# Optimization experiments

Hardware: AMD Instinct MI355X
Metric: run time of the kernel (lower is better)

## Reference

```python
import jax, jax.numpy as jnp
import numpy as np

B, S, DD, DE, DA = 32, 2048, 1024, 1024, 1024
NEG = -1000000000.0


def setup_inputs() -> dict:
    key = jax.random.key(0)
    k1, k2, k3, k4, k5 = jax.random.split(key, 5)
    query_state = jax.random.normal(k1, (B, DD), dtype=jnp.float32)
    encoder_hidden_states = jax.random.normal(k2, (B, S, DE), dtype=jnp.float32)
    attention_mask = jax.random.randint(k3, (B, S), 0, 2, dtype=jnp.int32)
    # W_c: Linear(DD+DE -> DA, bias=False): weight shape [DA, DD+DE]
    W_c = jax.random.normal(k4, (DA, DD + DE), dtype=jnp.float32) / np.sqrt(DD + DE)
    # V: Linear(DA -> 1, bias=False): weight shape [1, DA]
    V = jax.random.normal(k5, (1, DA), dtype=jnp.float32) / np.sqrt(DA)
    return {
        "query_state": query_state,
        "encoder_hidden_states": encoder_hidden_states,
        "attention_mask": attention_mask,
        "W_c": W_c,
        "V": V,
    }


def reference(query_state, encoder_hidden_states, attention_mask, W_c, V):
    # Split W_c along input dim: cat([q, e]) @ W_c.T == q @ Wq.T + e @ We.T
    Wq = W_c[:, :DD]          # [DA, DD]
    We = W_c[:, DD:]          # [DA, DE]
    q_proj = jnp.einsum('bd,ad->ba', query_state, Wq)            # [B, DA]
    e_proj = jnp.einsum('bsd,ad->bsa', encoder_hidden_states, We)  # [B, S, DA]
    energies = jnp.tanh(q_proj[:, None, :] + e_proj)             # [B, S, DA]
    scores = jnp.einsum('bsa,a->bs', energies, V[0])             # [B, S]
    scores = jnp.where(attention_mask == 0, NEG, scores)
    attention_weights = jax.nn.softmax(scores, axis=1)           # [B, S]
    context_vector = jnp.einsum('bs,bsd->bd', attention_weights, encoder_hidden_states)
    return context_vector, attention_weights
```

## Files before the change

kernel.cpp:

```cpp
#include <hip/hip_runtime.h>
#include <hip/hip_bf16.h>

#define NB 32
#define NS 2048
#define NDD 1024
#define NDE 1024
#define NDA 1024
#define NEGV (-1000000000.0f)

typedef __attribute__((ext_vector_type(8))) __bf16 bf16x8;
typedef __attribute__((ext_vector_type(4))) float f32x4;

__device__ __forceinline__ float fast_tanh(float x) {
    x = fminf(10.0f, fmaxf(-10.0f, x));
    float e = __expf(2.0f * x);
    return __fdividef(e - 1.0f, e + 1.0f);
}

__device__ __forceinline__ float bfu2f(unsigned short v) {
    union { unsigned u; float f; } c; c.u = (unsigned)v << 16; return c.f;
}

__global__ void prep_we(const float* __restrict__ Wc, __bf16* __restrict__ We) {
    int f = blockIdx.x * 256 + threadIdx.x;
    int a  = f >> 8;
    int k4 = f & 255;
    float4 v = *reinterpret_cast<const float4*>(Wc + (size_t)a * (NDD + NDE) + NDD + k4 * 4);
    union { __bf16 h[4]; uint2 u; } pk;
    pk.h[0] = (__bf16)v.x; pk.h[1] = (__bf16)v.y;
    pk.h[2] = (__bf16)v.z; pk.h[3] = (__bf16)v.w;
    *reinterpret_cast<uint2*>(We + (size_t)a * NDE + k4 * 4) = pk.u;
}

__global__ void prep_e(const float* __restrict__ E, __bf16* __restrict__ Eb) {
    size_t i = ((size_t)blockIdx.x * 256 + threadIdx.x) * 8;
    f32x4 x = __builtin_nontemporal_load(reinterpret_cast<const f32x4*>(E + i));
    f32x4 y = __builtin_nontemporal_load(reinterpret_cast<const f32x4*>(E + i + 4));
    union { __bf16 h[8]; uint4 u; } pk;
    pk.h[0] = (__bf16)x[0]; pk.h[1] = (__bf16)x[1]; pk.h[2] = (__bf16)x[2]; pk.h[3] = (__bf16)x[3];
    pk.h[4] = (__bf16)y[0]; pk.h[5] = (__bf16)y[1]; pk.h[6] = (__bf16)y[2]; pk.h[7] = (__bf16)y[3];
    *reinterpret_cast<uint4*>(Eb + i) = pk.u;
}

__global__ void qproj_kernel(const float* __restrict__ q, const float* __restrict__ Wc,
                             float* __restrict__ qp) {
    __shared__ float qs[NDD];
    int b = blockIdx.y;
    int a = blockIdx.x * 256 + threadIdx.x;
    float4 qv = *reinterpret_cast<const float4*>(q + (size_t)b * NDD + threadIdx.x * 4);
    *reinterpret_cast<float4*>(qs + threadIdx.x * 4) = qv;
    __syncthreads();
    const float* wrow = Wc + (size_t)a * (NDD + NDE);
    float acc = 0.f;
#pragma unroll 4
    for (int k4 = 0; k4 < 256; ++k4) {
        float4 w = *reinterpret_cast<const float4*>(wrow + k4 * 4);
        acc += qs[k4*4+0] * w.x + qs[k4*4+1] * w.y + qs[k4*4+2] * w.z + qs[k4*4+3] * w.w;
    }
    qp[(size_t)b * NDA + a] = acc;
}

__global__ __launch_bounds__(512, 2) void score256(
    const __bf16* __restrict__ Eb, const __bf16* __restrict__ We,
    const float* __restrict__ qp, const float* __restrict__ Vv,
    float* __restrict__ sp) {
    __shared__ __align__(16) __bf16 As[2][256 * 64];
    __shared__ __align__(16) __bf16 Bs[2][256 * 64];

    const int tid  = threadIdx.x;
    const int lane = tid & 63;
    const int l15  = lane & 15;
    const int h    = lane >> 4;
    const int wid  = tid >> 6;
    const int wr   = wid >> 2;
    const int wc   = wid & 3;

    const int bid = blockIdx.x;
    const int xcd = bid & 7;
    const int j   = bid >> 3;
    const int m   = xcd * 32 + (j >> 2);
    const int n   = j & 3;
    const int row0  = m * 256;
    const int ncol0 = n * 256;
    const int b     = m >> 3;

    f32x4 acc[8][4];
#pragma unroll
    for (int mf = 0; mf < 8; ++mf)
#pragma unroll
        for (int nf = 0; nf < 4; ++nf)
            acc[mf][nf] = (f32x4){0.f, 0.f, 0.f, 0.f};

    int offE[4], offW[4];
#pragma unroll
    for (int i = 0; i < 4; ++i) {
        int rr = i * 64 + (tid >> 3);
        int sg = (tid & 7) ^ (rr & 7);
        offE[i] = (row0  + rr) * 1024 + sg * 8;
        offW[i] = (ncol0 + rr) * 1024 + sg * 8;
    }

    const int slot0 = ((h ^ (l15 & 7)) * 16);
    const int aoffl = (wr * 128 + l15) * 128 + slot0;
    const int boffl = (wc * 64  + l15) * 128 + slot0;

#define STAGE8(abuf, bbuf, kc)                                                          \
    {                                                                                   \
        _Pragma("unroll")                                                               \
        for (int i = 0; i < 4; ++i)                                                     \
            __builtin_amdgcn_global_load_lds(                                           \
                (const __attribute__((address_space(1))) unsigned*)(Eb + offE[i] + (kc)),\
                (__attribute__((address_space(3))) unsigned*)((char*)(abuf) + i * 8192 + wid * 1024), \
                16, 0, 0);                                                              \
        _Pragma("unroll")                                                               \
        for (int i = 0; i < 4; ++i)                                                     \
            __builtin_amdgcn_global_load_lds(                                           \
                (const __attribute__((address_space(1))) unsigned*)(We + offW[i] + (kc)),\
                (__attribute__((address_space(3))) unsigned*)((char*)(bbuf) + i * 8192 + wid * 1024), \
                16, 0, 0);                                                              \
    }

    STAGE8(&As[0][0], &Bs[0][0], 0)
    __syncthreads();

    for (int T = 0; T < 16; ++T) {
        const int cur = T & 1;
        const char* Ab = (const char*)&As[cur][0];
        const char* Bb = (const char*)&Bs[cur][0];
        if (T < 15) STAGE8(&As[cur ^ 1][0], &Bs[cur ^ 1][0], (T + 1) * 64)

        bf16x8 bfr[4][2], afr[4][2];
#pragma unroll
        for (int nf = 0; nf < 4; ++nf) {
            bfr[nf][0] = *reinterpret_cast<const bf16x8*>(Bb + (boffl + nf * 2048));
            bfr[nf][1] = *reinterpret_cast<const bf16x8*>(Bb + ((boffl + nf * 2048) ^ 64));
        }
#pragma unroll
        for (int mi = 0; mi < 4; ++mi) {
            afr[mi][0] = *reinterpret_cast<const bf16x8*>(Ab + (aoffl + mi * 2048));
            afr[mi][1] = *reinterpret_cast<const bf16x8*>(Ab + ((aoffl + mi * 2048) ^ 64));
        }
        __builtin_amdgcn_s_setprio(1);
#pragma unroll
        for (int ks = 0; ks < 2; ++ks)
#pragma unroll
            for (int mi = 0; mi < 4; ++mi)
#pragma unroll
                for (int nf = 0; nf < 4; ++nf)
                    acc[mi][nf] = __builtin_amdgcn_mfma_f32_16x16x32_bf16(afr[mi][ks], bfr[nf][ks], acc[mi][nf], 0, 0, 0);
        __builtin_amdgcn_s_setprio(0);
#pragma unroll
        for (int mi = 0; mi < 4; ++mi) {
            afr[mi][0] = *reinterpret_cast<const bf16x8*>(Ab + (aoffl + (4 + mi) * 2048));
            afr[mi][1] = *reinterpret_cast<const bf16x8*>(Ab + ((aoffl + (4 + mi) * 2048) ^ 64));
        }
        __builtin_amdgcn_s_setprio(1);
#pragma unroll
        for (int ks = 0; ks < 2; ++ks)
#pragma unroll
            for (int mi = 0; mi < 4; ++mi)
#pragma unroll
                for (int nf = 0; nf < 4; ++nf)
                    acc[4 + mi][nf] = __builtin_amdgcn_mfma_f32_16x16x32_bf16(afr[mi][ks], bfr[nf][ks], acc[4 + mi][nf], 0, 0, 0);
        __builtin_amdgcn_s_setprio(0);
        __syncthreads();
    }

    float qv[4], vv[4];
#pragma unroll
    for (int nf = 0; nf < 4; ++nf) {
        int col = ncol0 + wc * 64 + nf * 16 + l15;
        qv[nf] = qp[(size_t)b * NDA + col];
        vv[nf] = Vv[col];
    }
    float* ps2 = reinterpret_cast<float*>(&As[0][0]);
#pragma unroll
    for (int mf = 0; mf < 8; ++mf)
#pragma unroll
        for (int jj = 0; jj < 4; ++jj) {
            float s = 0.f;
#pragma unroll
            for (int nf = 0; nf < 4; ++nf)
                s += fast_tanh(qv[nf] + acc[mf][nf][jj]) * vv[nf];
            s += __shfl_xor(s, 1);
            s += __shfl_xor(s, 2);
            s += __shfl_xor(s, 4);
            s += __shfl_xor(s, 8);
            if (l15 == 0)
                ps2[(wr * 128 + mf * 16 + h * 4 + jj) * 4 + wc] = s;
        }
    __syncthreads();
    if (tid < 256)
        sp[(size_t)n * (NB * NS) + row0 + tid] =
            ps2[tid * 4] + ps2[tid * 4 + 1] + ps2[tid * 4 + 2] + ps2[tid * 4 + 3];
}

__global__ void softmax_kernel(const float* __restrict__ sp, const int* __restrict__ mask,
                               float* __restrict__ wout, int np) {
    int b = blockIdx.x;
    const int* mrow = mask + (size_t)b * NS;
    float v[8];
    float lmax = -INFINITY;
#pragma unroll
    for (int jj = 0; jj < 8; ++jj) {
        int s = threadIdx.x + 256 * jj;
        float sc = 0.f;
        for (int nn = 0; nn < np; ++nn) sc += sp[(size_t)nn * (NB * NS) + b * NS + s];
        v[jj] = (mrow[s] == 0) ? NEGV : sc;
        lmax = fmaxf(lmax, v[jj]);
    }
#pragma unroll
    for (int mm = 1; mm <= 32; mm <<= 1) lmax = fmaxf(lmax, __shfl_xor(lmax, mm));
    __shared__ float redm[4], reds[4];
    if ((threadIdx.x & 63) == 0) redm[threadIdx.x >> 6] = lmax;
    __syncthreads();
    float bmax = fmaxf(fmaxf(redm[0], redm[1]), fmaxf(redm[2], redm[3]));
    float lsum = 0.f;
#pragma unroll
    for (int jj = 0; jj < 8; ++jj) { v[jj] = __expf(v[jj] - bmax); lsum += v[jj]; }
#pragma unroll
    for (int mm = 1; mm <= 32; mm <<= 1) lsum += __shfl_xor(lsum, mm);
    if ((threadIdx.x & 63) == 0) reds[threadIdx.x >> 6] = lsum;
    __syncthreads();
    float inv = __fdividef(1.0f, reds[0] + reds[1] + reds[2] + reds[3]);
#pragma unroll
    for (int jj = 0; jj < 8; ++jj) wout[(size_t)b * NS + threadIdx.x + 256 * jj] = v[jj] * inv;
}

__global__ void context_bf16(const __bf16* __restrict__ Eb, const float* __restrict__ w,
                             float* __restrict__ ctx) {
    int b  = blockIdx.x >> 3;
    int dc = blockIdx.x & 7;
    int dg = threadIdx.x & 31;
    int ss = threadIdx.x >> 5;
    const __bf16* base = Eb + (size_t)b * NS * NDE + (size_t)(ss * 256) * NDE + dc * 128 + dg * 4;
    const float* wb = w + (size_t)b * NS + ss * 256;
    float a0 = 0.f, a1 = 0.f, a2 = 0.f, a3 = 0.f;
#pragma unroll 8
    for (int s = 0; s < 256; ++s) {
        float ws = wb[s];
        uint2 u = *reinterpret_cast<const uint2*>(base + (size_t)s * NDE);
        a0 = fmaf(ws, bfu2f((unsigned short)(u.x & 0xffff)), a0);
        a1 = fmaf(ws, bfu2f((unsigned short)(u.x >> 16)), a1);
        a2 = fmaf(ws, bfu2f((unsigned short)(u.y & 0xffff)), a2);
        a3 = fmaf(ws, bfu2f((unsigned short)(u.y >> 16)), a3);
    }
    __shared__ float4 part[256];
    part[threadIdx.x] = make_float4(a0, a1, a2, a3);
    __syncthreads();
    if (threadIdx.x < 32) {
        float4 r = part[threadIdx.x];
#pragma unroll
        for (int k = 1; k < 8; ++k) {
            float4 p = part[threadIdx.x + 32 * k];
            r.x += p.x; r.y += p.y; r.z += p.z; r.w += p.w;
        }
        *reinterpret_cast<float4*>(ctx + (size_t)b * NDD + dc * 128 + threadIdx.x * 4) = r;
    }
}

extern "C" void kernel_launch(void* const* d_in, const int* in_sizes, int n_in,
                              void* d_out, int out_size, void* d_ws, size_t ws_size,
                              hipStream_t stream) {
    const float* query = (const float*)d_in[0];
    const float* enc   = (const float*)d_in[1];
    const int*   mask  = (const int*)d_in[2];
    const float* Wc    = (const float*)d_in[3];
    const float* V     = (const float*)d_in[4];

    float* out = (float*)d_out;
    float* ctx = out;
    float* wts = out + NB * NDD;

    const size_t WE_B = (size_t)NDA * NDE * 2;
    const size_t QP_B = (size_t)NB * NDA * 4;
    const size_t SP_B = (size_t)8 * NB * NS * 4;
    char* ws = (char*)d_ws;
    __bf16* We = (__bf16*)ws;
    float*  qp = (float*)(ws + WE_B);
    float*  sp = (float*)(ws + WE_B + QP_B);
    __bf16* Eb = (__bf16*)(ws + WE_B + QP_B + SP_B);

    hipLaunchKernelGGL(prep_we,      dim3(1024),  dim3(256), 0, stream, Wc, We);
    hipLaunchKernelGGL(qproj_kernel, dim3(4, NB), dim3(256), 0, stream, query, Wc, qp);
    hipLaunchKernelGGL(prep_e,       dim3(32768), dim3(256), 0, stream, enc, Eb);
    hipLaunchKernelGGL(score256,     dim3(1024),  dim3(512), 0, stream, Eb, We, qp, V, sp);
    hipLaunchKernelGGL(softmax_kernel, dim3(NB),  dim3(256), 0, stream, sp, mask, wts, 4);
    hipLaunchKernelGGL(context_bf16, dim3(256),   dim3(256), 0, stream, Eb, wts, ctx);
}
```

Baseline: 296.4 us.

## Deepen score GEMM pipeline to four K-stages with explicit vmcnt waits

The score GEMM main loop moves from two 64-wide K buffers to four 32-wide K buffers, so three loads are in flight ahead of compute. Synchronisation changes from __syncthreads to an explicit s_waitcnt vmcnt plus s_barrier, which lets outstanding async global-to-LDS loads stay pending across iterations. The LDS swizzle and the fragment offsets are recomputed for the narrower rows, and the min-blocks-per-SM hint of 2 on launch_bounds is dropped. The aim is to hide global load latency better. In exchange there is more barrier overhead per unit of K, and occupancy and register allocation may change.

```diff
diff --git a/kernel.cpp b/kernel.cpp
--- a/kernel.cpp
+++ b/kernel.cpp
@@ -60,12 +60,12 @@
     qp[(size_t)b * NDA + a] = acc;
 }
 
-__global__ __launch_bounds__(512, 2) void score256(
+__global__ __launch_bounds__(512) void score256(
     const __bf16* __restrict__ Eb, const __bf16* __restrict__ We,
     const float* __restrict__ qp, const float* __restrict__ Vv,
     float* __restrict__ sp) {
-    __shared__ __align__(16) __bf16 As[2][256 * 64];
-    __shared__ __align__(16) __bf16 Bs[2][256 * 64];
+    __shared__ __align__(16) __bf16 As[4][256 * 32];
+    __shared__ __align__(16) __bf16 Bs[4][256 * 32];
 
     const int tid  = threadIdx.x;
     const int lane = tid & 63;
@@ -91,80 +91,84 @@
         for (int nf = 0; nf < 4; ++nf)
             acc[mf][nf] = (f32x4){0.f, 0.f, 0.f, 0.f};
 
-    int offE[4], offW[4];
-#pragma unroll
-    for (int i = 0; i < 4; ++i) {
-        int rr = i * 64 + (tid >> 3);
-        int sg = (tid & 7) ^ (rr & 7);
-        offE[i] = (row0  + rr) * 1024 + sg * 8;
-        offW[i] = (ncol0 + rr) * 1024 + sg * 8;
-    }
-
-    const int slot0 = ((h ^ (l15 & 7)) * 16);
-    const int aoffl = (wr * 128 + l15) * 128 + slot0;
-    const int boffl = (wc * 64  + l15) * 128 + slot0;
-
-#define STAGE8(abuf, bbuf, kc)                                                          \
+    int offE[2], offW[2];
+#pragma unroll
+    for (int i = 0; i < 2; ++i) {
+        int chunk = i * 512 + tid;
+        int r  = chunk >> 2;
+        int sl = chunk & 3;
+        int sg = sl ^ ((r >> 1) & 3);
+        offE[i] = (row0  + r) * 1024 + sg * 8;
+        offW[i] = (ncol0 + r) * 1024 + sg * 8;
+    }
+
+    int aoff[8], boff[4];
+#pragma unroll
+    for (int mf = 0; mf < 8; ++mf) {
+        int r = wr * 128 + mf * 16 + l15;
+        aoff[mf] = r * 64 + ((h ^ ((r >> 1) & 3)) << 4);
+    }
+#pragma unroll
+    for (int nf = 0; nf < 4; ++nf) {
+        int r = wc * 64 + nf * 16 + l15;
+        boff[nf] = r * 64 + ((h ^ ((r >> 1) & 3)) << 4);
+    }
+
+#define STAGE(T)                                                                        \
     {                                                                                   \
-        _Pragma("unroll")                                                               \
-        for (int i = 0; i < 4; ++i)                                                     \
+        const int bufi = (T) & 3;                                                       \
+        const int kc   = (T) * 32;                                                      \
+        _Pragma("unroll")                                                               \
+        for (int i = 0; i < 2; ++i)                                                     \
             __builtin_amdgcn_global_load_lds(                                           \
-                (const __attribute__((address_space(1))) unsigned*)(Eb + offE[i] + (kc)),\
-                (__attribute__((address_space(3))) unsigned*)((char*)(abuf) + i * 8192 + wid * 1024), \
+                (const __attribute__((address_space(1))) unsigned*)(Eb + offE[i] + kc), \
+                (__attribute__((address_space(3))) unsigned*)((char*)&As[bufi][0] + i * 8192 + wid * 1024), \
                 16, 0, 0);                                                              \
         _Pragma("unroll")                                                               \
-        for (int i = 0; i < 4; ++i)                                                     \
+        for (int i = 0; i < 2; ++i)                                                     \
             __builtin_amdgcn_global_load_lds(                                           \
-                (const __attribute__((address_space(1))) unsigned*)(We + offW[i] + (kc)),\
-                (__attribute__((address_space(3))) unsigned*)((char*)(bbuf) + i * 8192 + wid * 1024), \
+                (const __attribute__((address_space(1))) unsigned*)(We + offW[i] + kc), \
+                (__attribute__((address_space(3))) unsigned*)((char*)&Bs[bufi][0] + i * 8192 + wid * 1024), \
                 16, 0, 0);                                                              \
     }
 
-    STAGE8(&As[0][0], &Bs[0][0], 0)
-    __syncthreads();
-
-    for (int T = 0; T < 16; ++T) {
-        const int cur = T & 1;
-        const char* Ab = (const char*)&As[cur][0];
-        const char* Bb = (const char*)&Bs[cur][0];
-        if (T < 15) STAGE8(&As[cur ^ 1][0], &Bs[cur ^ 1][0], (T + 1) * 64)
-
-        bf16x8 bfr[4][2], afr[4][2];
-#pragma unroll
-        for (int nf = 0; nf < 4; ++nf) {
-            bfr[nf][0] = *reinterpret_cast<const bf16x8*>(Bb + (boffl + nf * 2048));
-            bfr[nf][1] = *reinterpret_cast<const bf16x8*>(Bb + ((boffl + nf * 2048) ^ 64));
-        }
-#pragma unroll
-        for (int mi = 0; mi < 4; ++mi) {
-            afr[mi][0] = *reinterpret_cast<const bf16x8*>(Ab + (aoffl + mi * 2048));
-            afr[mi][1] = *reinterpret_cast<const bf16x8*>(Ab + ((aoffl + mi * 2048) ^ 64));
-        }
-        __builtin_amdgcn_s_setprio(1);
-#pragma unroll
-        for (int ks = 0; ks < 2; ++ks)
-#pragma unroll
-            for (int mi = 0; mi < 4; ++mi)
-#pragma unroll
-                for (int nf = 0; nf < 4; ++nf)
-                    acc[mi][nf] = __builtin_amdgcn_mfma_f32_16x16x32_bf16(afr[mi][ks], bfr[nf][ks], acc[mi][nf], 0, 0, 0);
-        __builtin_amdgcn_s_setprio(0);
-#pragma unroll
-        for (int mi = 0; mi < 4; ++mi) {
-            afr[mi][0] = *reinterpret_cast<const bf16x8*>(Ab + (aoffl + (4 + mi) * 2048));
-            afr[mi][1] = *reinterpret_cast<const bf16x8*>(Ab + ((aoffl + (4 + mi) * 2048) ^ 64));
-        }
-        __builtin_amdgcn_s_setprio(1);
-#pragma unroll
-        for (int ks = 0; ks < 2; ++ks)
-#pragma unroll
-            for (int mi = 0; mi < 4; ++mi)
-#pragma unroll
-                for (int nf = 0; nf < 4; ++nf)
-                    acc[4 + mi][nf] = __builtin_amdgcn_mfma_f32_16x16x32_bf16(afr[mi][ks], bfr[nf][ks], acc[4 + mi][nf], 0, 0, 0);
-        __builtin_amdgcn_s_setprio(0);
-        __syncthreads();
-    }
+#define COMPUTE(T)                                                                      \
+    {                                                                                   \
+        const char* Ab = (const char*)&As[(T) & 3][0];                                  \
+        const char* Bb = (const char*)&Bs[(T) & 3][0];                                  \
+        bf16x8 afr[8], bfr[4];                                                          \
+        _Pragma("unroll")                                                               \
+        for (int nf = 0; nf < 4; ++nf)                                                  \
+            bfr[nf] = *reinterpret_cast<const bf16x8*>(Bb + boff[nf]);                  \
+        _Pragma("unroll")                                                               \
+        for (int mf = 0; mf < 8; ++mf)                                                  \
+            afr[mf] = *reinterpret_cast<const bf16x8*>(Ab + aoff[mf]);                  \
+        __builtin_amdgcn_s_setprio(1);                                                  \
+        _Pragma("unroll")                                                               \
+        for (int mf = 0; mf < 8; ++mf)                                                  \
+            _Pragma("unroll")                                                           \
+            for (int nf = 0; nf < 4; ++nf)                                              \
+                acc[mf][nf] = __builtin_amdgcn_mfma_f32_16x16x32_bf16(afr[mf], bfr[nf], acc[mf][nf], 0, 0, 0); \
+        __builtin_amdgcn_s_setprio(0);                                                  \
+    }
+
+    STAGE(0) STAGE(1) STAGE(2)
+    asm volatile("s_waitcnt vmcnt(8)" ::: "memory");
+    __builtin_amdgcn_s_barrier();
+
+    for (int T = 0; T < 29; ++T) {
+        STAGE(T + 3)
+        COMPUTE(T)
+        asm volatile("s_waitcnt vmcnt(8)" ::: "memory");
+        __builtin_amdgcn_s_barrier();
+    }
+    COMPUTE(29)
+    asm volatile("s_waitcnt vmcnt(4)" ::: "memory");
+    __builtin_amdgcn_s_barrier();
+    COMPUTE(30)
+    asm volatile("s_waitcnt vmcnt(0)" ::: "memory");
+    __builtin_amdgcn_s_barrier();
+    COMPUTE(31)
 
     float qv[4], vv[4];
 #pragma unroll
```

Result: slower. 322.6 us (+8.8%).

## Split GEMM K-tile into four phases with interleaved half-stage async loads

Applied to the files above, without the earlier changes.

Restructures the double-buffered bf16 MFMA main loop into four sub-phases (A0xB01, A0xB23, A1xB23, A1xB01). Each phase issues half of the next tile's global-to-LDS loads and waits on partial vmcnt counts instead of staging everything up front and doing one full __syncthreads at the end. The goal is to spread memory traffic across the compute and overlap LDS reads, global loads and MFMAs more finely, in the style of a ping-pong schedule. In exchange it adds extra s_barriers per tile and hand-set waitcnt values that must match the load ordering exactly.

```diff
diff --git a/kernel.cpp b/kernel.cpp
--- a/kernel.cpp
+++ b/kernel.cpp
@@ -104,67 +104,93 @@
     const int aoffl = (wr * 128 + l15) * 128 + slot0;
     const int boffl = (wc * 64  + l15) * 128 + slot0;
 
-#define STAGE8(abuf, bbuf, kc)                                                          \
+#define S_HALF(SRC, OFFS, bufptr, kc, HALF)                                             \
     {                                                                                   \
         _Pragma("unroll")                                                               \
-        for (int i = 0; i < 4; ++i)                                                     \
+        for (int i = (HALF)*2; i < (HALF)*2 + 2; ++i)                                   \
             __builtin_amdgcn_global_load_lds(                                           \
-                (const __attribute__((address_space(1))) unsigned*)(Eb + offE[i] + (kc)),\
-                (__attribute__((address_space(3))) unsigned*)((char*)(abuf) + i * 8192 + wid * 1024), \
+                (const __attribute__((address_space(1))) unsigned*)(SRC + OFFS[i] + (kc)),\
+                (__attribute__((address_space(3))) unsigned*)((char*)(bufptr) + i * 8192 + wid * 1024), \
                 16, 0, 0);                                                              \
-        _Pragma("unroll")                                                               \
-        for (int i = 0; i < 4; ++i)                                                     \
-            __builtin_amdgcn_global_load_lds(                                           \
-                (const __attribute__((address_space(1))) unsigned*)(We + offW[i] + (kc)),\
-                (__attribute__((address_space(3))) unsigned*)((char*)(bbuf) + i * 8192 + wid * 1024), \
-                16, 0, 0);                                                              \
-    }
-
-    STAGE8(&As[0][0], &Bs[0][0], 0)
-    __syncthreads();
-
-    for (int T = 0; T < 16; ++T) {
-        const int cur = T & 1;
-        const char* Ab = (const char*)&As[cur][0];
-        const char* Bb = (const char*)&Bs[cur][0];
-        if (T < 15) STAGE8(&As[cur ^ 1][0], &Bs[cur ^ 1][0], (T + 1) * 64)
-
-        bf16x8 bfr[4][2], afr[4][2];
-#pragma unroll
-        for (int nf = 0; nf < 4; ++nf) {
-            bfr[nf][0] = *reinterpret_cast<const bf16x8*>(Bb + (boffl + nf * 2048));
-            bfr[nf][1] = *reinterpret_cast<const bf16x8*>(Bb + ((boffl + nf * 2048) ^ 64));
-        }
-#pragma unroll
-        for (int mi = 0; mi < 4; ++mi) {
-            afr[mi][0] = *reinterpret_cast<const bf16x8*>(Ab + (aoffl + mi * 2048));
-            afr[mi][1] = *reinterpret_cast<const bf16x8*>(Ab + ((aoffl + mi * 2048) ^ 64));
-        }
-        __builtin_amdgcn_s_setprio(1);
-#pragma unroll
-        for (int ks = 0; ks < 2; ++ks)
-#pragma unroll
-            for (int mi = 0; mi < 4; ++mi)
-#pragma unroll
-                for (int nf = 0; nf < 4; ++nf)
-                    acc[mi][nf] = __builtin_amdgcn_mfma_f32_16x16x32_bf16(afr[mi][ks], bfr[nf][ks], acc[mi][nf], 0, 0, 0);
-        __builtin_amdgcn_s_setprio(0);
-#pragma unroll
-        for (int mi = 0; mi < 4; ++mi) {
-            afr[mi][0] = *reinterpret_cast<const bf16x8*>(Ab + (aoffl + (4 + mi) * 2048));
-            afr[mi][1] = *reinterpret_cast<const bf16x8*>(Ab + ((aoffl + (4 + mi) * 2048) ^ 64));
-        }
-        __builtin_amdgcn_s_setprio(1);
-#pragma unroll
-        for (int ks = 0; ks < 2; ++ks)
-#pragma unroll
-            for (int mi = 0; mi < 4; ++mi)
-#pragma unroll
-                for (int nf = 0; nf < 4; ++nf)
-                    acc[4 + mi][nf] = __builtin_amdgcn_mfma_f32_16x16x32_bf16(afr[mi][ks], bfr[nf][ks], acc[4 + mi][nf], 0, 0, 0);
-        __builtin_amdgcn_s_setprio(0);
-        __syncthreads();
-    }
+    }
+
+#define RD_A(dst, base)                                                                 \
+    {                                                                                   \
+        _Pragma("unroll")                                                               \
+        for (int mi = 0; mi < 4; ++mi) {                                                \
+            dst[mi][0] = *reinterpret_cast<const bf16x8*>(Ab + (aoffl + ((base) + mi) * 2048)); \
+            dst[mi][1] = *reinterpret_cast<const bf16x8*>(Ab + ((aoffl + ((base) + mi) * 2048) ^ 64)); \
+        }                                                                               \
+    }
+
+#define MFMA16(ACCR, ACCC, AFR, BFR)                                                    \
+    {                                                                                   \
+        __builtin_amdgcn_s_setprio(1);                                                  \
+        _Pragma("unroll")                                                               \
+        for (int ks = 0; ks < 2; ++ks)                                                  \
+            _Pragma("unroll")                                                           \
+            for (int mi = 0; mi < 4; ++mi)                                              \
+                _Pragma("unroll")                                                       \
+                for (int ni = 0; ni < 2; ++ni)                                          \
+                    acc[(ACCR) + mi][(ACCC) + ni] = __builtin_amdgcn_mfma_f32_16x16x32_bf16( \
+                        AFR[mi][ks], BFR[ni][ks], acc[(ACCR) + mi][(ACCC) + ni], 0, 0, 0); \
+        __builtin_amdgcn_s_setprio(0);                                                  \
+    }
+
+#define DO_TILE(CUR, KCN, STG, G2STR, G1STR)                                            \
+    {                                                                                   \
+        const char* Ab = (const char*)&As[CUR][0];                                      \
+        const char* Bb = (const char*)&Bs[CUR][0];                                      \
+        __bf16* An = &As[(CUR) ^ 1][0];                                                 \
+        __bf16* Bn = &Bs[(CUR) ^ 1][0];                                                 \
+        bf16x8 afr[4][2], bfrA[2][2], bfrB[2][2];                                       \
+                                  \
+        RD_A(afr, 0)                                                                    \
+        _Pragma("unroll")                                                               \
+        for (int ni = 0; ni < 2; ++ni) {                                                \
+            bfrA[ni][0] = *reinterpret_cast<const bf16x8*>(Bb + (boffl + ni * 2048));   \
+            bfrA[ni][1] = *reinterpret_cast<const bf16x8*>(Bb + ((boffl + ni * 2048) ^ 64)); \
+        }                                                                               \
+        if (STG) S_HALF(Eb, offE, An, KCN, 0)                                           \
+        __builtin_amdgcn_s_barrier();                                                   \
+        MFMA16(0, 0, afr, bfrA)                                                         \
+        __builtin_amdgcn_s_barrier();                                                   \
+                                   \
+        _Pragma("unroll")                                                               \
+        for (int ni = 0; ni < 2; ++ni) {                                                \
+            bfrB[ni][0] = *reinterpret_cast<const bf16x8*>(Bb + (boffl + (2 + ni) * 2048)); \
+            bfrB[ni][1] = *reinterpret_cast<const bf16x8*>(Bb + ((boffl + (2 + ni) * 2048) ^ 64)); \
+        }                                                                               \
+        if (STG) S_HALF(We, offW, Bn, KCN, 0)                                           \
+        asm volatile("s_waitcnt vmcnt(" G2STR ")" ::: "memory");                        \
+        __builtin_amdgcn_s_barrier();                                                   \
+        MFMA16(0, 2, afr, bfrB)                                                         \
+        __builtin_amdgcn_s_barrier();                                                   \
+                                          \
+        RD_A(afr, 4)                                                                    \
+        if (STG) S_HALF(We, offW, Bn, KCN, 1)                                           \
+        __builtin_amdgcn_s_barrier();                                                   \
+        MFMA16(4, 2, afr, bfrB)                                                         \
+        __builtin_amdgcn_s_barrier();                                                   \
+                                               \
+        if (STG) S_HALF(Eb, offE, An, KCN, 1)                                           \
+        asm volatile("s_waitcnt vmcnt(" G1STR ")" ::: "memory");                        \
+        __builtin_amdgcn_s_barrier();                                                   \
+        MFMA16(4, 0, afr, bfrA)                                                         \
+        __builtin_amdgcn_s_barrier();                                                   \
+    }
+
+    S_HALF(Eb, offE, &As[0][0], 0, 0)
+    S_HALF(We, offW, &Bs[0][0], 0, 0)
+    S_HALF(We, offW, &Bs[0][0], 0, 1)
+    S_HALF(Eb, offE, &As[0][0], 0, 1)
+    asm volatile("s_waitcnt vmcnt(2)" ::: "memory");
+    __builtin_amdgcn_s_barrier();
+
+    for (int T = 0; T < 15; ++T) {
+        DO_TILE(T & 1, (T + 1) * 64, 1, "4", "2")
+    }
+    DO_TILE(1, 0, 0, "0", "0")
 
     float qv[4], vv[4];
 #pragma unroll
@@ -173,6 +199,7 @@
         qv[nf] = qp[(size_t)b * NDA + col];
         vv[nf] = Vv[col];
     }
+    __syncthreads();
     float* ps2 = reinterpret_cast<float*>(&As[0][0]);
 #pragma unroll
     for (int mf = 0; mf < 8; ++mf)
```

Result: no change. 296.6 us (+0.1%).

## Shrink score GEMM tile to 256x128 with 4 waves and BK=32

Applied to the files above, without the earlier changes.

Retiles the score GEMM from 256x256 output tiles with 8 waves and K-step 64 to 256x128 tiles with 4 waves and K-step 32. This doubles the grid to 2048 blocks and writes 8 partial score planes, so the softmax kernel now sums 8 partials instead of 4. The LDS swizzle changes to match the 64-byte rows. The goal is more blocks in flight and a smaller LDS footprint. The cost is that each E tile is loaded twice as often and the loop has more barriers per unit of work.

```diff
diff --git a/kernel.cpp b/kernel.cpp
--- a/kernel.cpp
+++ b/kernel.cpp
@@ -60,28 +60,28 @@
     qp[(size_t)b * NDA + a] = acc;
 }
 
-__global__ __launch_bounds__(512, 2) void score256(
+__global__ __launch_bounds__(256, 2) void score256(
     const __bf16* __restrict__ Eb, const __bf16* __restrict__ We,
     const float* __restrict__ qp, const float* __restrict__ Vv,
     float* __restrict__ sp) {
-    __shared__ __align__(16) __bf16 As[2][256 * 64];
-    __shared__ __align__(16) __bf16 Bs[2][256 * 64];
+    __shared__ __align__(16) __bf16 As[2][256 * 32];
+    __shared__ __align__(16) __bf16 Bs[2][128 * 32];
 
     const int tid  = threadIdx.x;
     const int lane = tid & 63;
     const int l15  = lane & 15;
     const int h    = lane >> 4;
     const int wid  = tid >> 6;
-    const int wr   = wid >> 2;
-    const int wc   = wid & 3;
+    const int wr   = wid >> 1;
+    const int wc   = wid & 1;
 
     const int bid = blockIdx.x;
     const int xcd = bid & 7;
     const int j   = bid >> 3;
-    const int m   = xcd * 32 + (j >> 2);
-    const int n   = j & 3;
+    const int m   = xcd * 32 + (j >> 3);
+    const int n   = j & 7;
     const int row0  = m * 256;
-    const int ncol0 = n * 256;
+    const int ncol0 = n * 128;
     const int b     = m >> 3;
 
     f32x4 acc[8][4];
@@ -91,78 +91,70 @@
         for (int nf = 0; nf < 4; ++nf)
             acc[mf][nf] = (f32x4){0.f, 0.f, 0.f, 0.f};
 
-    int offE[4], offW[4];
+    int offE[4], offW[2];
 #pragma unroll
     for (int i = 0; i < 4; ++i) {
-        int rr = i * 64 + (tid >> 3);
-        int sg = (tid & 7) ^ (rr & 7);
-        offE[i] = (row0  + rr) * 1024 + sg * 8;
-        offW[i] = (ncol0 + rr) * 1024 + sg * 8;
-    }
-
-    const int slot0 = ((h ^ (l15 & 7)) * 16);
-    const int aoffl = (wr * 128 + l15) * 128 + slot0;
-    const int boffl = (wc * 64  + l15) * 128 + slot0;
-
-#define STAGE8(abuf, bbuf, kc)                                                          \
+        int chunk = i * 256 + tid;
+        int r  = chunk >> 2;
+        int sg = (chunk & 3) ^ ((r >> 1) & 3);
+        offE[i] = (row0 + r) * 1024 + sg * 8;
+    }
+#pragma unroll
+    for (int i = 0; i < 2; ++i) {
+        int chunk = i * 256 + tid;
+        int r  = chunk >> 2;
+        int sg = (chunk & 3) ^ ((r >> 1) & 3);
+        offW[i] = (ncol0 + r) * 1024 + sg * 8;
+    }
+
+    int aoff[8], boff[4];
+#pragma unroll
+    for (int mf = 0; mf < 8; ++mf) {
+        int r = wr * 128 + mf * 16 + l15;
+        aoff[mf] = r * 64 + ((h ^ ((r >> 1) & 3)) << 4);
+    }
+#pragma unroll
+    for (int nf = 0; nf < 4; ++nf) {
+        int r = wc * 64 + nf * 16 + l15;
+        boff[nf] = r * 64 + ((h ^ ((r >> 1) & 3)) << 4);
+    }
+
+#define STAGE(buf, kc)                                                                  \
     {                                                                                   \
         _Pragma("unroll")                                                               \
         for (int i = 0; i < 4; ++i)                                                     \
             __builtin_amdgcn_global_load_lds(                                           \
                 (const __attribute__((address_space(1))) unsigned*)(Eb + offE[i] + (kc)),\
-                (__attribute__((address_space(3))) unsigned*)((char*)(abuf) + i * 8192 + wid * 1024), \
+                (__attribute__((address_space(3))) unsigned*)((char*)&As[buf][0] + i * 4096 + wid * 1024), \
                 16, 0, 0);                                                              \
         _Pragma("unroll")                                                               \
-        for (int i = 0; i < 4; ++i)                                                     \
+        for (int i = 0; i < 2; ++i)                                                     \
             __builtin_amdgcn_global_load_lds(                                           \
                 (const __attribute__((address_space(1))) unsigned*)(We + offW[i] + (kc)),\
-                (__attribute__((address_space(3))) unsigned*)((char*)(bbuf) + i * 8192 + wid * 1024), \
+                (__attribute__((address_space(3))) unsigned*)((char*)&Bs[buf][0] + i * 4096 + wid * 1024), \
                 16, 0, 0);                                                              \
     }
 
-    STAGE8(&As[0][0], &Bs[0][0], 0)
-    __syncthreads();
-
-    for (int T = 0; T < 16; ++T) {
-        const int cur = T & 1;
+    STAGE(0, 0)
+    __syncthreads();
+
+    for (int it = 0; it < 32; ++it) {
+        const int cur = it & 1;
+        if (it < 31) STAGE(cur ^ 1, (it + 1) * 32)
         const char* Ab = (const char*)&As[cur][0];
         const char* Bb = (const char*)&Bs[cur][0];
-        if (T < 15) STAGE8(&As[cur ^ 1][0], &Bs[cur ^ 1][0], (T + 1) * 64)
-
-        bf16x8 bfr[4][2], afr[4][2];
-#pragma unroll
-        for (int nf = 0; nf < 4; ++nf) {
-            bfr[nf][0] = *reinterpret_cast<const bf16x8*>(Bb + (boffl + nf * 2048));
-            bfr[nf][1] = *reinterpret_cast<const bf16x8*>(Bb + ((boffl + nf * 2048) ^ 64));
-        }
-#pragma unroll
-        for (int mi = 0; mi < 4; ++mi) {
-            afr[mi][0] = *reinterpret_cast<const bf16x8*>(Ab + (aoffl + mi * 2048));
-            afr[mi][1] = *reinterpret_cast<const bf16x8*>(Ab + ((aoffl + mi * 2048) ^ 64));
-        }
-        __builtin_amdgcn_s_setprio(1);
-#pragma unroll
-        for (int ks = 0; ks < 2; ++ks)
-#pragma unroll
-            for (int mi = 0; mi < 4; ++mi)
-#pragma unroll
-                for (int nf = 0; nf < 4; ++nf)
-                    acc[mi][nf] = __builtin_amdgcn_mfma_f32_16x16x32_bf16(afr[mi][ks], bfr[nf][ks], acc[mi][nf], 0, 0, 0);
-        __builtin_amdgcn_s_setprio(0);
-#pragma unroll
-        for (int mi = 0; mi < 4; ++mi) {
-            afr[mi][0] = *reinterpret_cast<const bf16x8*>(Ab + (aoffl + (4 + mi) * 2048));
-            afr[mi][1] = *reinterpret_cast<const bf16x8*>(Ab + ((aoffl + (4 + mi) * 2048) ^ 64));
-        }
-        __builtin_amdgcn_s_setprio(1);
-#pragma unroll
-        for (int ks = 0; ks < 2; ++ks)
-#pragma unroll
-            for (int mi = 0; mi < 4; ++mi)
-#pragma unroll
-                for (int nf = 0; nf < 4; ++nf)
-                    acc[4 + mi][nf] = __builtin_amdgcn_mfma_f32_16x16x32_bf16(afr[mi][ks], bfr[nf][ks], acc[4 + mi][nf], 0, 0, 0);
-        __builtin_amdgcn_s_setprio(0);
+        bf16x8 bfr[4], afr[8];
+#pragma unroll
+        for (int nf = 0; nf < 4; ++nf)
+            bfr[nf] = *reinterpret_cast<const bf16x8*>(Bb + boff[nf]);
+#pragma unroll
+        for (int mf = 0; mf < 8; ++mf)
+            afr[mf] = *reinterpret_cast<const bf16x8*>(Ab + aoff[mf]);
+#pragma unroll
+        for (int mf = 0; mf < 8; ++mf)
+#pragma unroll
+            for (int nf = 0; nf < 4; ++nf)
+                acc[mf][nf] = __builtin_amdgcn_mfma_f32_16x16x32_bf16(afr[mf], bfr[nf], acc[mf][nf], 0, 0, 0);
         __syncthreads();
     }
 
@@ -173,7 +165,7 @@
         qv[nf] = qp[(size_t)b * NDA + col];
         vv[nf] = Vv[col];
     }
-    float* ps2 = reinterpret_cast<float*>(&As[0][0]);
+    float* ps = reinterpret_cast<float*>(&As[0][0]);
 #pragma unroll
     for (int mf = 0; mf < 8; ++mf)
 #pragma unroll
@@ -187,12 +179,11 @@
             s += __shfl_xor(s, 4);
             s += __shfl_xor(s, 8);
             if (l15 == 0)
-                ps2[(wr * 128 + mf * 16 + h * 4 + jj) * 4 + wc] = s;
+                ps[(wr * 128 + mf * 16 + h * 4 + jj) * 2 + wc] = s;
         }
     __syncthreads();
     if (tid < 256)
-        sp[(size_t)n * (NB * NS) + row0 + tid] =
-            ps2[tid * 4] + ps2[tid * 4 + 1] + ps2[tid * 4 + 2] + ps2[tid * 4 + 3];
+        sp[(size_t)n * (NB * NS) + row0 + tid] = ps[tid * 2] + ps[tid * 2 + 1];
 }
 
 __global__ void softmax_kernel(const float* __restrict__ sp, const int* __restrict__ mask,
@@ -284,7 +275,7 @@
     hipLaunchKernelGGL(prep_we,      dim3(1024),  dim3(256), 0, stream, Wc, We);
     hipLaunchKernelGGL(qproj_kernel, dim3(4, NB), dim3(256), 0, stream, query, Wc, qp);
     hipLaunchKernelGGL(prep_e,       dim3(32768), dim3(256), 0, stream, enc, Eb);
-    hipLaunchKernelGGL(score256,     dim3(1024),  dim3(512), 0, stream, Eb, We, qp, V, sp);
-    hipLaunchKernelGGL(softmax_kernel, dim3(NB),  dim3(256), 0, stream, sp, mask, wts, 4);
+    hipLaunchKernelGGL(score256,     dim3(2048),  dim3(256), 0, stream, Eb, We, qp, V, sp);
+    hipLaunchKernelGGL(softmax_kernel, dim3(NB),  dim3(256), 0, stream, sp, mask, wts, 8);
     hipLaunchKernelGGL(context_bf16, dim3(256),   dim3(256), 0, stream, Eb, wts, ctx);
 }
```

Result: slower. 343.1 us (+15.7%).
